# Kernel tuning notes

Hardware: AMD Instinct MI355X
Metric: run time of the kernel (lower is better)

Reference implementation:

```python
import math
import jax, jax.numpy as jnp
import numpy as np

B = 8192           # batch_size
N = 256            # num_features (n_tokens)
D = 64             # embedding_dim (even)
H = D // 2         # half dim for sin/cos coefficients


def setup_inputs() -> dict:
    key = jax.random.key(0)
    k1, k2, k3 = jax.random.split(key, 3)
    inputs = jax.random.normal(k1, (B, N), dtype=jnp.float32)
    # coef initialized with stddev=sigma (sigma=1.0)
    coef = jax.random.normal(k2, (1, N, H), dtype=jnp.float32)
    weight = jax.random.normal(k3, (1, N, D, D), dtype=jnp.float32)
    bias = jnp.zeros((1, N, D), dtype=jnp.float32)
    return {"inputs": inputs, "coef": coef, "weight": weight, "bias": bias}


def reference(inputs, coef, weight, bias):
    # v: [B, N, H]
    v = (2.0 * math.pi) * coef * inputs[..., None]
    emb = jnp.concatenate([jnp.sin(v), jnp.cos(v)], axis=-1)  # [B, N, D]
    # per-token linear: one DxD matmul per token (NLinear), done as batched einsum
    emb = jnp.einsum('bni,nio->bno', emb, weight[0]) + bias    # [B, N, D]
    emb = jax.nn.relu(emb)
    return emb.reshape(-1, N * D)                              # [B, N*D]
```

## Files before the change

### kernel.cpp

```cpp
#include <hip/hip_runtime.h>


typedef short bf16x8 __attribute__((ext_vector_type(8)));
typedef float f32x4 __attribute__((ext_vector_type(4)));

#define BM    128
#define TILES 4
#define LDW   72

__device__ __forceinline__ short f2bf(float f) {
    unsigned u = __float_as_uint(f);
    unsigned r = (u + 0x7FFFu + ((u >> 16) & 1u)) >> 16;
    return (short)r;
}

__global__ __launch_bounds__(256) void pe_kernel(
    const float* __restrict__ x,
    const float* __restrict__ coef,
    const float* __restrict__ wgt,
    const float* __restrict__ bias,
    float* __restrict__ out)
{
    const int N = 256;

    const int bid = blockIdx.x;
    const int xcd = bid & 7;
    const int j   = bid >> 3;
    const int n      = xcd * 32 + (j & 31);
    const int b_base = (j >> 5) * (BM * TILES);

    __shared__ short wtl[64 * LDW];
    const int t = threadIdx.x;

    const float* Wn = wgt + n * 4096;
    #pragma unroll
    for (int it = 0; it < 16; ++it) {
        int idx = it * 256 + t;
        int i = idx >> 6, o = idx & 63;
        wtl[o * LDW + i] = f2bf(Wn[idx]);
    }
    __syncthreads();

    const int w  = t >> 6;
    const int l  = t & 63;
    const int lr = l & 15;
    const int lg = l >> 4;

    bf16x8 bfr[4][2];
    #pragma unroll
    for (int nf = 0; nf < 4; ++nf)
        #pragma unroll
        for (int ki = 0; ki < 2; ++ki)
            bfr[nf][ki] = *(const bf16x8*)(&wtl[(nf * 16 + lr) * LDW + ki * 32 + lg * 8]);

    const float* cp = coef + n * 32 + lg * 8;
    float c[8];
    #pragma unroll
    for (int jj = 0; jj < 8; ++jj) c[jj] = cp[jj];

    const float* bn = bias + n * 64;
    f32x4 bv[4];
    #pragma unroll
    for (int nf = 0; nf < 4; ++nf)
        bv[nf] = *(const f32x4*)(bn + nf * 16 + lg * 4);

    for (int tt = 0; tt < TILES; ++tt) {
        const int b0   = b_base + tt * BM;
        const int row0 = b0 + w * 32 + lr;
        const float x0 = x[row0 * N + n];
        const float x1 = x[(row0 + 16) * N + n];

        bf16x8 a_s[2], a_c[2];
        #pragma unroll
        for (int m = 0; m < 2; ++m) {
            float xv = m ? x1 : x0;
            #pragma unroll
            for (int jj = 0; jj < 8; ++jj) {
                float v = c[jj] * xv;
                v = __builtin_amdgcn_fractf(v);
                a_s[m][jj] = f2bf(__builtin_amdgcn_sinf(v));
                a_c[m][jj] = f2bf(__builtin_amdgcn_cosf(v));
            }
        }

        f32x4 acc[2][4];
        #pragma unroll
        for (int m = 0; m < 2; ++m)
            #pragma unroll
            for (int nf = 0; nf < 4; ++nf) {
                f32x4 z = {0.f, 0.f, 0.f, 0.f};
                z = __builtin_amdgcn_mfma_f32_16x16x32_bf16(bfr[nf][0], a_s[m], z, 0, 0, 0);
                z = __builtin_amdgcn_mfma_f32_16x16x32_bf16(bfr[nf][1], a_c[m], z, 0, 0, 0);
                acc[m][nf] = z;
            }

        #pragma unroll
        for (int m = 0; m < 2; ++m) {
            int row = b0 + w * 32 + m * 16 + lr;
            float* op = out + (size_t)row * 16384 + n * 64 + lg * 4;
            #pragma unroll
            for (int nf = 0; nf < 4; ++nf) {
                f32x4 v = acc[m][nf] + bv[nf];
                f32x4 r;
                #pragma unroll
                for (int q = 0; q < 4; ++q) r[q] = fmaxf(v[q], 0.0f);
                *(f32x4*)(op + nf * 16) = r;
            }
        }
    }
}

extern "C" void kernel_launch(void* const* d_in, const int* in_sizes, int n_in,
                              void* d_out, int out_size, void* d_ws, size_t ws_size,
                              hipStream_t stream) {
    const float* x    = (const float*)d_in[0];
    const float* coef = (const float*)d_in[1];
    const float* wgt  = (const float*)d_in[2];
    const float* bias = (const float*)d_in[3];
    float* out = (float*)d_out;

    dim3 grid(256 * (8192 / (BM * TILES)));
    dim3 block(256);
    hipLaunchKernelGGL(pe_kernel, grid, block, 0, stream,
                       x, coef, wgt, bias, out);
}
```

Before: 111.7 us.

## Tile blocks over four consecutive tokens per batch-row slab instead of four batch tiles

Each block now handles 128 batch rows across four adjacent tokens, staging all four tokens' weight matrices in shared memory, where before it handled one token across 512 batch rows. Each output row a block writes becomes 1 KB of contiguous memory instead of 256 B, which improves write locality, and the x reads for adjacent tokens fall in the same cache lines. In exchange, each block converts four times as much weight data to bf16, and the weights get reloaded by 64 row-slab blocks instead of 16. Shared memory per block also grows fourfold, and the XCD-aware block-to-token mapping is dropped.

```diff
diff --git a/kernel.cpp b/kernel.cpp
--- a/kernel.cpp
+++ b/kernel.cpp
@@ -4,9 +4,9 @@
 typedef short bf16x8 __attribute__((ext_vector_type(8)));
 typedef float f32x4 __attribute__((ext_vector_type(4)));
 
-#define BM    128
-#define TILES 4
-#define LDW   72
+#define ROWS 128
+#define TT   4
+#define LDW  72
 
 __device__ __forceinline__ short f2bf(float f) {
     unsigned u = __float_as_uint(f);
@@ -24,20 +24,19 @@
     const int N = 256;
 
     const int bid = blockIdx.x;
-    const int xcd = bid & 7;
-    const int j   = bid >> 3;
-    const int n      = xcd * 32 + (j & 31);
-    const int b_base = (j >> 5) * (BM * TILES);
+    const int n0  = (bid & 63) * TT;
+    const int b0g = (bid >> 6) * ROWS;
 
-    __shared__ short wtl[64 * LDW];
+    __shared__ short wtl[TT][64 * LDW];
     const int t = threadIdx.x;
 
-    const float* Wn = wgt + n * 4096;
     #pragma unroll
-    for (int it = 0; it < 16; ++it) {
+    for (int it = 0; it < 64; ++it) {
         int idx = it * 256 + t;
-        int i = idx >> 6, o = idx & 63;
-        wtl[o * LDW + i] = f2bf(Wn[idx]);
+        int nt  = idx >> 12;
+        int rem = idx & 4095;
+        int i = rem >> 6, o = rem & 63;
+        wtl[nt][o * LDW + i] = f2bf(wgt[(n0 + nt) * 4096 + rem]);
     }
     __syncthreads();
 
@@ -45,28 +44,29 @@
     const int l  = t & 63;
     const int lr = l & 15;
     const int lg = l >> 4;
+    const int row0 = b0g + w * 32 + lr;
 
-    bf16x8 bfr[4][2];
-    #pragma unroll
-    for (int nf = 0; nf < 4; ++nf)
+    for (int nt = 0; nt < TT; ++nt) {
+        const int n = n0 + nt;
+
+        bf16x8 bfr[4][2];
         #pragma unroll
-        for (int ki = 0; ki < 2; ++ki)
-            bfr[nf][ki] = *(const bf16x8*)(&wtl[(nf * 16 + lr) * LDW + ki * 32 + lg * 8]);
+        for (int nf = 0; nf < 4; ++nf)
+            #pragma unroll
+            for (int ki = 0; ki < 2; ++ki)
+                bfr[nf][ki] = *(const bf16x8*)(&wtl[nt][(nf * 16 + lr) * LDW + ki * 32 + lg * 8]);
 
-    const float* cp = coef + n * 32 + lg * 8;
-    float c[8];
-    #pragma unroll
-    for (int jj = 0; jj < 8; ++jj) c[jj] = cp[jj];
+        const float* cp = coef + n * 32 + lg * 8;
+        float c[8];
+        #pragma unroll
+        for (int jj = 0; jj < 8; ++jj) c[jj] = cp[jj];
 
-    const float* bn = bias + n * 64;
-    f32x4 bv[4];
-    #pragma unroll
-    for (int nf = 0; nf < 4; ++nf)
-        bv[nf] = *(const f32x4*)(bn + nf * 16 + lg * 4);
+        const float* bn = bias + n * 64;
+        f32x4 bv[4];
+        #pragma unroll
+        for (int nf = 0; nf < 4; ++nf)
+            bv[nf] = *(const f32x4*)(bn + nf * 16 + lg * 4);
 
-    for (int tt = 0; tt < TILES; ++tt) {
-        const int b0   = b_base + tt * BM;
-        const int row0 = b0 + w * 32 + lr;
         const float x0 = x[row0 * N + n];
         const float x1 = x[(row0 + 16) * N + n];
 
@@ -96,7 +96,7 @@
 
         #pragma unroll
         for (int m = 0; m < 2; ++m) {
-            int row = b0 + w * 32 + m * 16 + lr;
+            int row = b0g + w * 32 + m * 16 + lr;
             float* op = out + (size_t)row * 16384 + n * 64 + lg * 4;
             #pragma unroll
             for (int nf = 0; nf < 4; ++nf) {
@@ -119,7 +119,7 @@
     const float* bias = (const float*)d_in[3];
     float* out = (float*)d_out;
 
-    dim3 grid(256 * (8192 / (BM * TILES)));
+    dim3 grid((8192 / ROWS) * (256 / TT));
     dim3 block(256);
     hipLaunchKernelGGL(pe_kernel, grid, block, 0, stream,
                        x, coef, wgt, bias, out);
```

After: 117.8 us. 1.05x slower.
